# Performance work log

Hardware: AMD Instinct MI355X
Metric: run time of the kernel (lower is better)

## Reference

```python
import jax, jax.numpy as jnp
import numpy as np

B, H, W, D = 8, 64, 64, 1024


def setup_inputs() -> dict:
    key = jax.random.key(0)
    ks = jax.random.split(key, 10)
    s = 0.02
    return {
        "x": jax.random.normal(ks[0], (B, H, W, D), dtype=jnp.float32),
        "Wq": jax.random.normal(ks[1], (D, D), dtype=jnp.float32) * s,
        "bq": jnp.zeros((D,), dtype=jnp.float32),
        "Wk": jax.random.normal(ks[2], (D, D), dtype=jnp.float32) * s,
        "bk": jnp.zeros((D,), dtype=jnp.float32),
        "Wv": jax.random.normal(ks[3], (D, D), dtype=jnp.float32) * s,
        "bv": jnp.zeros((D,), dtype=jnp.float32),
        "Wo": jax.random.normal(ks[4], (D, D), dtype=jnp.float32) * s,
        "bo": jnp.zeros((D,), dtype=jnp.float32),
        "sigma": jnp.ones((1,), dtype=jnp.float32),
    }


def _dist(n, dtype):
    i = jnp.arange(n)
    return jnp.square(i[:, None] - i[None, :]).astype(dtype)


def reference(x, Wq, bq, Wk, bk, Wv, bv, Wo, bo, sigma):
    b, h, w, d = x.shape
    gw = 1.0 / (2.0 * jnp.square(sigma))  # scalar (shape [1])
    q = jnp.einsum('bhwd,ed->bhwe', x, Wq) + bq
    k = jnp.einsum('bhwd,ed->bhwe', x, Wk) + bk
    v = jnp.einsum('bhwd,ed->bhwe', x, Wv) + bv
    # row attention: attend across width within each row
    r_qk = jnp.einsum('bhwd,bhkd->bhwk', q, k) - gw[0] * _dist(w, x.dtype)
    r_attn = jax.nn.softmax(r_qk, axis=-1)               # [b,h,w,w]
    r_out = jnp.einsum('bhwk,bhkd->bhwd', r_attn, v)
    # column attention: attend across height within each column
    c_qk = jnp.einsum('bhwd,bgwd->bwhg', q, k) - gw[0] * _dist(h, x.dtype)
    c_attn = jax.nn.softmax(c_qk, axis=-1)               # [b,w,h,h]
    c_out = jnp.einsum('bwhg,bgwd->bhwd', c_attn, v)
    out = r_out + c_out
    return jnp.einsum('bhwd,ed->bhwe', out, Wo) + bo
```

## Files before the change

### kernel.cpp

```cpp
#include <hip/hip_runtime.h>


typedef _Float16 f16;
typedef __attribute__((ext_vector_type(8))) _Float16 f16x8;
typedef __attribute__((ext_vector_type(4))) float f32x4;

#define DEV __device__ __forceinline__

__global__ __launch_bounds__(256) void k_cvt_f16(const float* __restrict__ in,
                                                 f16* __restrict__ out, int n8) {
  int stride = gridDim.x * blockDim.x;
  for (int i = blockIdx.x * blockDim.x + threadIdx.x; i < n8; i += stride) {
    const float4* p = (const float4*)in + (size_t)i * 2;
    float4 a = p[0];
    float4 b = p[1];
    f16x8 o;
    o[0] = (f16)a.x; o[1] = (f16)a.y; o[2] = (f16)a.z; o[3] = (f16)a.w;
    o[4] = (f16)b.x; o[5] = (f16)b.y; o[6] = (f16)b.z; o[7] = (f16)b.w;
    *(f16x8*)(out + (size_t)i * 8) = o;
  }
}

template<bool C_F32>
__global__ __launch_bounds__(512, 2) void k_gemm256(const f16* __restrict__ A,
                                                    const f16* __restrict__ B,
                                                    const float* __restrict__ b0,
                                                    const float* __restrict__ b1,
                                                    const float* __restrict__ b2,
                                                    void* __restrict__ Cout,
                                                    int M, int N, int K) {
  __shared__ f16 smem[2][2][2][128 * 64];

  const int tid = threadIdx.x;
  const int lane = tid & 63;
  const int wid = tid >> 6;
  const int wr = wid >> 2;
  const int wc = wid & 3;
  const int lane_r = lane & 15;
  const int g = lane >> 4;

  const int nwg = gridDim.x;
  const int bid = blockIdx.x;
  const int swz = (bid & 7) * (nwg >> 3) + (bid >> 3);
  const int nbn = N >> 8;
  const int bm = swz / nbn, bn = swz % nbn;

  const int u0 = ((g) ^ (lane_r & 7)) * 8;
  const int u1 = ((4 + g) ^ (lane_r & 7)) * 8;
  const int arow = lane >> 3;
  const int acol = ((lane & 7) ^ (lane >> 3)) * 8;

  const f16* Ag[2] = { A + (size_t)(bm * 256) * K, A + (size_t)(bm * 256 + 128) * K };
  const f16* Bg[2] = { B + (size_t)(bn * 256) * K, B + (size_t)(bn * 256 + 128) * K };

  f32x4 acc[8][4];
#pragma unroll
  for (int i = 0; i < 8; ++i)
#pragma unroll
    for (int j = 0; j < 4; ++j) acc[i][j] = (f32x4){0.f, 0.f, 0.f, 0.f};

#define STAGE(gbase, kt, lbase)                                                     \
  {                                                                                 \
    _Pragma("unroll") for (int i_ = 0; i_ < 2; ++i_) {                              \
      const f16* g_ = (gbase) + (size_t)(wid * 16 + i_ * 8 + arow) * K + (kt) * 64 + acol; \
      __builtin_amdgcn_global_load_lds(                                             \
          (const __attribute__((address_space(1))) void*)g_,                        \
          (__attribute__((address_space(3))) void*)((lbase) + (wid * 16 + i_ * 8) * 64), \
          16, 0, 0);                                                                \
    }                                                                               \
  }

#define MFMAQ(q)                                                                    \
  _Pragma("unroll") for (int mm = 0; mm < 2; ++mm)                                  \
  _Pragma("unroll") for (int n = 0; n < 4; ++n) {                                   \
    acc[(q)*2 + mm][n] = __builtin_amdgcn_mfma_f32_16x16x32_f16(afrag[mm][0], bfrag[n][0], acc[(q)*2 + mm][n], 0, 0, 0); \
    acc[(q)*2 + mm][n] = __builtin_amdgcn_mfma_f32_16x16x32_f16(afrag[mm][1], bfrag[n][1], acc[(q)*2 + mm][n], 0, 0, 0); \
  }

#define READ_A(q)                                                                   \
  _Pragma("unroll") for (int mm = 0; mm < 2; ++mm) {                                \
    const int rb_ = ((q)*32 + mm * 16 + lane_r) * 64;                               \
    afrag[mm][0] = *(const f16x8*)&As_[rb_ + u0];                                   \
    afrag[mm][1] = *(const f16x8*)&As_[rb_ + u1];                                   \
  }

#define KTILE(t, slot, mode)                                                        \
  {                                                                                 \
    f16* As_ = smem[slot][0][wr];                                                   \
    f16* Bs_ = smem[slot][1][wc >> 1];                                              \
    f16x8 bfrag[4][2], afrag[2][2];                                                 \
    _Pragma("unroll") for (int n = 0; n < 4; ++n) {                                 \
      const int rb_ = ((wc & 1) * 64 + n * 16 + lane_r) * 64;                       \
      bfrag[n][0] = *(const f16x8*)&Bs_[rb_ + u0];                                  \
      bfrag[n][1] = *(const f16x8*)&Bs_[rb_ + u1];                                  \
    }                                                                               \
    READ_A(0)                                                                       \
    if ((mode) >= 1) STAGE(Ag[0], (t) + 1, smem[(slot) ^ 1][0][0]);                 \
    asm volatile("s_waitcnt lgkmcnt(8)" ::: "memory");                              \
    __builtin_amdgcn_s_barrier();                                                   \
    asm volatile("s_waitcnt lgkmcnt(0)" ::: "memory");                              \
    __builtin_amdgcn_s_setprio(1);                                                  \
    MFMAQ(0)                                                                        \
    __builtin_amdgcn_s_setprio(0);                                                  \
    __builtin_amdgcn_s_barrier();                                                   \
    READ_A(1)                                                                       \
    if ((mode) >= 1) STAGE(Ag[1], (t) + 1, smem[(slot) ^ 1][0][1]);                 \
    __builtin_amdgcn_s_barrier();                                                   \
    asm volatile("s_waitcnt lgkmcnt(0)" ::: "memory");                              \
    __builtin_amdgcn_s_setprio(1);                                                  \
    MFMAQ(1)                                                                        \
    __builtin_amdgcn_s_setprio(0);                                                  \
    __builtin_amdgcn_s_barrier();                                                   \
    READ_A(2)                                                                       \
    if ((mode) == 2) STAGE(Bg[0], (t) + 2, smem[slot][1][0]);                       \
    __builtin_amdgcn_s_barrier();                                                   \
    asm volatile("s_waitcnt lgkmcnt(0)" ::: "memory");                              \
    __builtin_amdgcn_s_setprio(1);                                                  \
    MFMAQ(2)                                                                        \
    __builtin_amdgcn_s_setprio(0);                                                  \
    __builtin_amdgcn_s_barrier();                                                   \
    READ_A(3)                                                                       \
    if ((mode) == 2) STAGE(Bg[1], (t) + 2, smem[slot][1][1]);                       \
    if ((mode) == 2) { asm volatile("s_waitcnt vmcnt(4)" ::: "memory"); }           \
    else if ((mode) == 1) { asm volatile("s_waitcnt vmcnt(0)" ::: "memory"); }      \
    __builtin_amdgcn_s_barrier();                                                   \
    asm volatile("s_waitcnt lgkmcnt(0)" ::: "memory");                              \
    __builtin_amdgcn_s_setprio(1);                                                  \
    MFMAQ(3)                                                                        \
    __builtin_amdgcn_s_setprio(0);                                                  \
    __builtin_amdgcn_s_barrier();                                                   \
  }

  const int nt = K >> 6;

  STAGE(Ag[0], 0, smem[0][0][0]);
  STAGE(Ag[1], 0, smem[0][0][1]);
  STAGE(Bg[0], 0, smem[0][1][0]);
  STAGE(Bg[1], 0, smem[0][1][1]);
  STAGE(Bg[0], 1, smem[1][1][0]);
  STAGE(Bg[1], 1, smem[1][1][1]);
  asm volatile("s_waitcnt vmcnt(4)" ::: "memory");
  __builtin_amdgcn_s_barrier();

  for (int t = 0; t + 3 < nt; t += 2) {
    KTILE(t, 0, 2)
    KTILE(t + 1, 1, 2)
  }
  KTILE(nt - 2, 0, 1)
  KTILE(nt - 1, 1, 0)

  const int mrow0 = bm * 256 + wr * 128 + (lane >> 4) * 4;
  const int ncol0 = bn * 256 + wc * 64 + (lane & 15);
#pragma unroll
  for (int n = 0; n < 4; ++n) {
    const int col = ncol0 + n * 16;
    const float* bp = (col < 1024) ? b0 : ((col < 2048) ? b1 : b2);
    const float bvv = bp[col & 1023];
#pragma unroll
    for (int mrep = 0; mrep < 8; ++mrep) {
#pragma unroll
      for (int r = 0; r < 4; ++r) {
        const int row = mrow0 + mrep * 16 + r;
        const float val = acc[mrep][n][r] + bvv;
        if (C_F32) ((float*)Cout)[(size_t)row * N + col] = val;
        else       ((f16*)Cout)[(size_t)row * N + col] = (f16)val;
      }
    }
  }
#undef KTILE
#undef READ_A
#undef MFMAQ
#undef STAGE
}

template<bool IS_COL>
__global__ __launch_bounds__(256) void k_attn(const f16* __restrict__ qkv,
                                              f16* __restrict__ attn,
                                              const float* __restrict__ sigma) {
  __shared__ union { float S[64][68]; f16 Vt[256][72]; } sm;
  __shared__ f16 P[64][72];

  const int tid = threadIdx.x;
  const int lane = tid & 63;
  const int wid = tid >> 6;
  const int blk = blockIdx.x;

  size_t tok0; int tstr;
  if (IS_COL) { tok0 = (size_t)(blk >> 6) * 4096 + (blk & 63); tstr = 64; }
  else        { tok0 = (size_t)blk * 64;                       tstr = 1;  }
  const size_t ibase = tok0 * 3072;  const int  istr = tstr * 3072;
  const size_t obase = tok0 * 1024;  const int  ostr = tstr * 1024;

  const float sg = sigma[0];
  const float gw = 0.5f / (sg * sg);

  const int m0 = wid * 16;
  const int lr = lane & 15;
  const int lq = lane >> 4;

  f32x4 sacc[4];
#pragma unroll
  for (int nt = 0; nt < 4; ++nt) sacc[nt] = (f32x4){0.f, 0.f, 0.f, 0.f};
  const f16* qp = qkv + ibase + (size_t)(m0 + lr) * istr + lq * 8;
  const f16* kp = qkv + ibase + 1024 + (size_t)lr * istr + lq * 8;
#pragma unroll 2
  for (int ks = 0; ks < 32; ++ks) {
    f16x8 af = *(const f16x8*)(qp + ks * 32);
#pragma unroll
    for (int nt = 0; nt < 4; ++nt) {
      f16x8 bfr = *(const f16x8*)(kp + (size_t)nt * 16 * istr + ks * 32);
      sacc[nt] = __builtin_amdgcn_mfma_f32_16x16x32_f16(af, bfr, sacc[nt], 0, 0, 0);
    }
  }
#pragma unroll
  for (int nt = 0; nt < 4; ++nt)
#pragma unroll
    for (int r = 0; r < 4; ++r) {
      const int row = m0 + lq * 4 + r;
      const int col = nt * 16 + lr;
      const float dd = (float)(row - col);
      sm.S[row][col] = sacc[nt][r] - gw * dd * dd;
    }
  __syncthreads();

  {
    const int r = tid >> 2, s4 = tid & 3;
    const float4* sp = (const float4*)&sm.S[r][s4 * 16];
    float vals[16];
#pragma unroll
    for (int j = 0; j < 4; ++j) {
      float4 t = sp[j];
      vals[j * 4 + 0] = t.x; vals[j * 4 + 1] = t.y; vals[j * 4 + 2] = t.z; vals[j * 4 + 3] = t.w;
    }
    float mx = vals[0];
#pragma unroll
    for (int j = 1; j < 16; ++j) mx = fmaxf(mx, vals[j]);
    mx = fmaxf(mx, __shfl_xor(mx, 1));
    mx = fmaxf(mx, __shfl_xor(mx, 2));
    float sum = 0.f;
#pragma unroll
    for (int j = 0; j < 16; ++j) { vals[j] = __expf(vals[j] - mx); sum += vals[j]; }
    sum += __shfl_xor(sum, 1);
    sum += __shfl_xor(sum, 2);
    const float inv = 1.f / sum;
#pragma unroll
    for (int j = 0; j < 16; ++j) P[r][s4 * 16 + j] = (f16)(vals[j] * inv);
  }
  __syncthreads();

  const f16x8 af0 = *(const f16x8*)&P[m0 + lr][lq * 8];
  const f16x8 af1 = *(const f16x8*)&P[m0 + lr][32 + lq * 8];

  const int kr = tid & 63;
  const int cg = tid >> 6;
  const f16* vp = qkv + ibase + 2048 + (size_t)kr * istr;

  for (int c = 0; c < 4; ++c) {
#pragma unroll
    for (int j8 = 0; j8 < 8; ++j8) {
      const int cl = cg * 64 + j8 * 8;
      f16x8 vv = *(const f16x8*)(vp + c * 256 + cl);
#pragma unroll
      for (int e = 0; e < 8; ++e) sm.Vt[cl + e][kr] = vv[e];
    }
    __syncthreads();
#pragma unroll
    for (int nt = 0; nt < 16; ++nt) {
      const f16x8 bf0 = *(const f16x8*)&sm.Vt[nt * 16 + lr][lq * 8];
      const f16x8 bf1 = *(const f16x8*)&sm.Vt[nt * 16 + lr][32 + lq * 8];
      f32x4 o = (f32x4){0.f, 0.f, 0.f, 0.f};
      o = __builtin_amdgcn_mfma_f32_16x16x32_f16(af0, bf0, o, 0, 0, 0);
      o = __builtin_amdgcn_mfma_f32_16x16x32_f16(af1, bf1, o, 0, 0, 0);
#pragma unroll
      for (int r = 0; r < 4; ++r) {
        const int row = m0 + lq * 4 + r;
        const int col = c * 256 + nt * 16 + lr;
        const size_t addr = obase + (size_t)row * ostr + col;
        float val = o[r];
        if (IS_COL) val += (float)attn[addr];
        attn[addr] = (f16)val;
      }
    }
    __syncthreads();
  }
}

extern "C" void kernel_launch(void* const* d_in, const int* in_sizes, int n_in,
                              void* d_out, int out_size, void* d_ws, size_t ws_size,
                              hipStream_t stream) {
  const float* x  = (const float*)d_in[0];
  const float* Wq = (const float*)d_in[1];
  const float* bq = (const float*)d_in[2];
  const float* Wk = (const float*)d_in[3];
  const float* bk = (const float*)d_in[4];
  const float* Wv = (const float*)d_in[5];
  const float* bv = (const float*)d_in[6];
  const float* Wo = (const float*)d_in[7];
  const float* bo = (const float*)d_in[8];
  const float* sg = (const float*)d_in[9];

  const int M = 8 * 64 * 64;
  const size_t NE = (size_t)M * 1024;

  f16* xb   = (f16*)d_ws;
  f16* wqkv = xb + NE;
  f16* wob  = wqkv + 3 * 1024 * 1024;
  f16* qkv  = wob + 1024 * 1024;

  k_cvt_f16<<<2048, 256, 0, stream>>>(x, xb, (int)(NE / 8));
  k_cvt_f16<<<256, 256, 0, stream>>>(Wq, wqkv,                   (1024 * 1024) / 8);
  k_cvt_f16<<<256, 256, 0, stream>>>(Wk, wqkv + 1024 * 1024,     (1024 * 1024) / 8);
  k_cvt_f16<<<256, 256, 0, stream>>>(Wv, wqkv + 2 * 1024 * 1024, (1024 * 1024) / 8);
  k_cvt_f16<<<256, 256, 0, stream>>>(Wo, wob,                    (1024 * 1024) / 8);

  k_gemm256<false><<<(M / 256) * (3072 / 256), 512, 0, stream>>>(
      xb, wqkv, bq, bk, bv, qkv, M, 3072, 1024);

  f16* attn = xb;
  k_attn<false><<<512, 256, 0, stream>>>(qkv, attn, sg);
  k_attn<true><<<512, 256, 0, stream>>>(qkv, attn, sg);

  k_gemm256<true><<<(M / 256) * (1024 / 256), 512, 0, stream>>>(
      attn, wob, bo, bo, bo, (float*)d_out, M, 1024, 1024);
}
```

Measured before the change: 523.6 us.

## Make GEMM persistent with cross-tile prefetch and merge conversion kernels

Turns the 256x256 GEMM into a persistent kernel with 256 workgroups, each looping over several output tiles. The next tile's first K-slices are prefetched during the last K-steps of the current tile, hiding the prologue and epilogue load latency. The five fp32-to-fp16 conversion launches are merged into one kernel to cut launch overhead. In exchange, the bid-swizzled tile ordering (bid&7 interleave) is dropped, which may hurt L2 reuse, and the epilogue stores are no longer overlapped across tiles.

```diff
diff --git a/kernel.cpp b/kernel.cpp
--- a/kernel.cpp
+++ b/kernel.cpp
@@ -5,19 +5,31 @@
 typedef __attribute__((ext_vector_type(8))) _Float16 f16x8;
 typedef __attribute__((ext_vector_type(4))) float f32x4;
 
-#define DEV __device__ __forceinline__
-
-__global__ __launch_bounds__(256) void k_cvt_f16(const float* __restrict__ in,
-                                                 f16* __restrict__ out, int n8) {
-  int stride = gridDim.x * blockDim.x;
-  for (int i = blockIdx.x * blockDim.x + threadIdx.x; i < n8; i += stride) {
-    const float4* p = (const float4*)in + (size_t)i * 2;
-    float4 a = p[0];
-    float4 b = p[1];
+__global__ __launch_bounds__(256) void k_cvt_all(
+    const float* __restrict__ x, const float* __restrict__ Wq,
+    const float* __restrict__ Wk, const float* __restrict__ Wv,
+    const float* __restrict__ Wo, f16* __restrict__ xb,
+    f16* __restrict__ wqkv, f16* __restrict__ wob) {
+  const int stride = gridDim.x * blockDim.x;
+  const int X8 = 33554432 / 8;
+  const int W8 = 1048576 / 8;
+  const int total = X8 + 4 * W8;
+  for (int i = blockIdx.x * blockDim.x + threadIdx.x; i < total; i += stride) {
+    const float* src; f16* dst; int o8;
+    if (i < X8) { src = x; dst = xb; o8 = i; }
+    else {
+      int j = i - X8; int seg = j >> 17; o8 = j & (W8 - 1);
+      if (seg == 0)      { src = Wq; dst = wqkv; }
+      else if (seg == 1) { src = Wk; dst = wqkv + 1048576; }
+      else if (seg == 2) { src = Wv; dst = wqkv + 2097152; }
+      else               { src = Wo; dst = wob; }
+    }
+    const float4* p = (const float4*)src + (size_t)o8 * 2;
+    float4 a = p[0]; float4 b = p[1];
     f16x8 o;
-    o[0] = (f16)a.x; o[1] = (f16)a.y; o[2] = (f16)a.z; o[3] = (f16)a.w;
-    o[4] = (f16)b.x; o[5] = (f16)b.y; o[6] = (f16)b.z; o[7] = (f16)b.w;
-    *(f16x8*)(out + (size_t)i * 8) = o;
+    o[0]=(f16)a.x; o[1]=(f16)a.y; o[2]=(f16)a.z; o[3]=(f16)a.w;
+    o[4]=(f16)b.x; o[5]=(f16)b.y; o[6]=(f16)b.z; o[7]=(f16)b.w;
+    *(f16x8*)(dst + (size_t)o8 * 8) = o;
   }
 }
 
@@ -28,7 +40,7 @@
                                                     const float* __restrict__ b1,
                                                     const float* __restrict__ b2,
                                                     void* __restrict__ Cout,
-                                                    int M, int N, int K) {
+                                                    int M, int N, int K, int ntiles) {
   __shared__ f16 smem[2][2][2][128 * 64];
 
   const int tid = threadIdx.x;
@@ -39,19 +51,10 @@
   const int lane_r = lane & 15;
   const int g = lane >> 4;
 
-  const int nwg = gridDim.x;
-  const int bid = blockIdx.x;
-  const int swz = (bid & 7) * (nwg >> 3) + (bid >> 3);
-  const int nbn = N >> 8;
-  const int bm = swz / nbn, bn = swz % nbn;
-
   const int u0 = ((g) ^ (lane_r & 7)) * 8;
   const int u1 = ((4 + g) ^ (lane_r & 7)) * 8;
   const int arow = lane >> 3;
   const int acol = ((lane & 7) ^ (lane >> 3)) * 8;
-
-  const f16* Ag[2] = { A + (size_t)(bm * 256) * K, A + (size_t)(bm * 256 + 128) * K };
-  const f16* Bg[2] = { B + (size_t)(bn * 256) * K, B + (size_t)(bn * 256 + 128) * K };
 
   f32x4 acc[8][4];
 #pragma unroll
@@ -84,7 +87,7 @@
     afrag[mm][1] = *(const f16x8*)&As_[rb_ + u1];                                   \
   }
 
-#define KTILE(t, slot, mode)                                                        \
+#define KTILE(slot, mode, AgP0, AgP1, ktA, BgP0, BgP1, ktB)                         \
   {                                                                                 \
     f16* As_ = smem[slot][0][wr];                                                   \
     f16* Bs_ = smem[slot][1][wc >> 1];                                              \
@@ -95,7 +98,7 @@
       bfrag[n][1] = *(const f16x8*)&Bs_[rb_ + u1];                                  \
     }                                                                               \
     READ_A(0)                                                                       \
-    if ((mode) >= 1) STAGE(Ag[0], (t) + 1, smem[(slot) ^ 1][0][0]);                 \
+    if ((mode) >= 1) STAGE(AgP0, ktA, smem[(slot) ^ 1][0][0]);                      \
     asm volatile("s_waitcnt lgkmcnt(8)" ::: "memory");                              \
     __builtin_amdgcn_s_barrier();                                                   \
     asm volatile("s_waitcnt lgkmcnt(0)" ::: "memory");                              \
@@ -104,7 +107,7 @@
     __builtin_amdgcn_s_setprio(0);                                                  \
     __builtin_amdgcn_s_barrier();                                                   \
     READ_A(1)                                                                       \
-    if ((mode) >= 1) STAGE(Ag[1], (t) + 1, smem[(slot) ^ 1][0][1]);                 \
+    if ((mode) >= 1) STAGE(AgP1, ktA, smem[(slot) ^ 1][0][1]);                      \
     __builtin_amdgcn_s_barrier();                                                   \
     asm volatile("s_waitcnt lgkmcnt(0)" ::: "memory");                              \
     __builtin_amdgcn_s_setprio(1);                                                  \
@@ -112,7 +115,7 @@
     __builtin_amdgcn_s_setprio(0);                                                  \
     __builtin_amdgcn_s_barrier();                                                   \
     READ_A(2)                                                                       \
-    if ((mode) == 2) STAGE(Bg[0], (t) + 2, smem[slot][1][0]);                       \
+    if ((mode) == 2) STAGE(BgP0, ktB, smem[slot][1][0]);                            \
     __builtin_amdgcn_s_barrier();                                                   \
     asm volatile("s_waitcnt lgkmcnt(0)" ::: "memory");                              \
     __builtin_amdgcn_s_setprio(1);                                                  \
@@ -120,7 +123,7 @@
     __builtin_amdgcn_s_setprio(0);                                                  \
     __builtin_amdgcn_s_barrier();                                                   \
     READ_A(3)                                                                       \
-    if ((mode) == 2) STAGE(Bg[1], (t) + 2, smem[slot][1][1]);                       \
+    if ((mode) == 2) STAGE(BgP1, ktB, smem[slot][1][1]);                            \
     if ((mode) == 2) { asm volatile("s_waitcnt vmcnt(4)" ::: "memory"); }           \
     else if ((mode) == 1) { asm volatile("s_waitcnt vmcnt(0)" ::: "memory"); }      \
     __builtin_amdgcn_s_barrier();                                                   \
@@ -131,41 +134,68 @@
     __builtin_amdgcn_s_barrier();                                                   \
   }
 
-  const int nt = K >> 6;
-
-  STAGE(Ag[0], 0, smem[0][0][0]);
-  STAGE(Ag[1], 0, smem[0][0][1]);
-  STAGE(Bg[0], 0, smem[0][1][0]);
-  STAGE(Bg[1], 0, smem[0][1][1]);
-  STAGE(Bg[0], 1, smem[1][1][0]);
-  STAGE(Bg[1], 1, smem[1][1][1]);
+  const int nbn = N >> 8;
+  const int NT = K >> 6;
+
+  int tidx = blockIdx.x;
+  const f16 *AgC0, *AgC1, *BgC0, *BgC1;
+  {
+    int bm = tidx / nbn, bn = tidx % nbn;
+    AgC0 = A + (size_t)(bm * 256) * K;  AgC1 = AgC0 + (size_t)128 * K;
+    BgC0 = B + (size_t)(bn * 256) * K;  BgC1 = BgC0 + (size_t)128 * K;
+  }
+
+  STAGE(AgC0, 0, smem[0][0][0]);
+  STAGE(AgC1, 0, smem[0][0][1]);
+  STAGE(BgC0, 0, smem[0][1][0]);
+  STAGE(BgC1, 0, smem[0][1][1]);
+  STAGE(BgC0, 1, smem[1][1][0]);
+  STAGE(BgC1, 1, smem[1][1][1]);
   asm volatile("s_waitcnt vmcnt(4)" ::: "memory");
   __builtin_amdgcn_s_barrier();
 
-  for (int t = 0; t + 3 < nt; t += 2) {
-    KTILE(t, 0, 2)
-    KTILE(t + 1, 1, 2)
-  }
-  KTILE(nt - 2, 0, 1)
-  KTILE(nt - 1, 1, 0)
-
-  const int mrow0 = bm * 256 + wr * 128 + (lane >> 4) * 4;
-  const int ncol0 = bn * 256 + wc * 64 + (lane & 15);
-#pragma unroll
-  for (int n = 0; n < 4; ++n) {
-    const int col = ncol0 + n * 16;
-    const float* bp = (col < 1024) ? b0 : ((col < 2048) ? b1 : b2);
-    const float bvv = bp[col & 1023];
-#pragma unroll
-    for (int mrep = 0; mrep < 8; ++mrep) {
-#pragma unroll
-      for (int r = 0; r < 4; ++r) {
-        const int row = mrow0 + mrep * 16 + r;
-        const float val = acc[mrep][n][r] + bvv;
-        if (C_F32) ((float*)Cout)[(size_t)row * N + col] = val;
-        else       ((f16*)Cout)[(size_t)row * N + col] = (f16)val;
+  for (int i = 0; i < ntiles; ++i) {
+    const f16 *AgN0 = AgC0, *AgN1 = AgC1, *BgN0 = BgC0, *BgN1 = BgC1;
+    const int nidx = tidx + gridDim.x;
+    if (i + 1 < ntiles) {
+      int bm = nidx / nbn, bn = nidx % nbn;
+      AgN0 = A + (size_t)(bm * 256) * K;  AgN1 = AgN0 + (size_t)128 * K;
+      BgN0 = B + (size_t)(bn * 256) * K;  BgN1 = BgN0 + (size_t)128 * K;
+    }
+    for (int t = 0; t + 3 < NT; t += 2) {
+      KTILE(0, 2, AgC0, AgC1, t + 1, BgC0, BgC1, t + 2)
+      KTILE(1, 2, AgC0, AgC1, t + 2, BgC0, BgC1, t + 3)
+    }
+    if (i + 1 < ntiles) {
+      KTILE(0, 2, AgC0, AgC1, NT - 1, BgN0, BgN1, 0)
+      KTILE(1, 2, AgN0, AgN1, 0,      BgN0, BgN1, 1)
+    } else {
+      KTILE(0, 1, AgC0, AgC1, NT - 1, BgC0, BgC1, 0)
+      KTILE(1, 0, AgC0, AgC1, 0,      BgC0, BgC1, 0)
+    }
+    {
+      const int bm = tidx / nbn, bn = tidx % nbn;
+      const int mrow0 = bm * 256 + wr * 128 + (lane >> 4) * 4;
+      const int ncol0 = bn * 256 + wc * 64 + (lane & 15);
+#pragma unroll
+      for (int n = 0; n < 4; ++n) {
+        const int col = ncol0 + n * 16;
+        const float* bp = (col < 1024) ? b0 : ((col < 2048) ? b1 : b2);
+        const float bvv = bp[col & 1023];
+#pragma unroll
+        for (int mrep = 0; mrep < 8; ++mrep) {
+#pragma unroll
+          for (int r = 0; r < 4; ++r) {
+            const int row = mrow0 + mrep * 16 + r;
+            const float val = acc[mrep][n][r] + bvv;
+            if (C_F32) ((float*)Cout)[(size_t)row * N + col] = val;
+            else       ((f16*)Cout)[(size_t)row * N + col] = (f16)val;
+            acc[mrep][n][r] = 0.f;
+          }
+        }
       }
     }
+    tidx = nidx; AgC0 = AgN0; AgC1 = AgN1; BgC0 = BgN0; BgC1 = BgN1;
   }
 #undef KTILE
 #undef READ_A
@@ -188,8 +218,8 @@
   size_t tok0; int tstr;
   if (IS_COL) { tok0 = (size_t)(blk >> 6) * 4096 + (blk & 63); tstr = 64; }
   else        { tok0 = (size_t)blk * 64;                       tstr = 1;  }
-  const size_t ibase = tok0 * 3072;  const int  istr = tstr * 3072;
-  const size_t obase = tok0 * 1024;  const int  ostr = tstr * 1024;
+  const size_t ibase = tok0 * 3072;  const int istr = tstr * 3072;
+  const size_t obase = tok0 * 1024;  const int ostr = tstr * 1024;
 
   const float sg = sigma[0];
   const float gw = 0.5f / (sg * sg);
@@ -307,19 +337,13 @@
   f16* wob  = wqkv + 3 * 1024 * 1024;
   f16* qkv  = wob + 1024 * 1024;
 
-  k_cvt_f16<<<2048, 256, 0, stream>>>(x, xb, (int)(NE / 8));
-  k_cvt_f16<<<256, 256, 0, stream>>>(Wq, wqkv,                   (1024 * 1024) / 8);
-  k_cvt_f16<<<256, 256, 0, stream>>>(Wk, wqkv + 1024 * 1024,     (1024 * 1024) / 8);
-  k_cvt_f16<<<256, 256, 0, stream>>>(Wv, wqkv + 2 * 1024 * 1024, (1024 * 1024) / 8);
-  k_cvt_f16<<<256, 256, 0, stream>>>(Wo, wob,                    (1024 * 1024) / 8);
-
-  k_gemm256<false><<<(M / 256) * (3072 / 256), 512, 0, stream>>>(
-      xb, wqkv, bq, bk, bv, qkv, M, 3072, 1024);
+  k_cvt_all<<<2048, 256, 0, stream>>>(x, Wq, Wk, Wv, Wo, xb, wqkv, wob);
+
+  k_gemm256<false><<<256, 512, 0, stream>>>(xb, wqkv, bq, bk, bv, qkv, M, 3072, 1024, 6);
 
   f16* attn = xb;
   k_attn<false><<<512, 256, 0, stream>>>(qkv, attn, sg);
   k_attn<true><<<512, 256, 0, stream>>>(qkv, attn, sg);
 
-  k_gemm256<true><<<(M / 256) * (1024 / 256), 512, 0, stream>>>(
-      attn, wob, bo, bo, bo, (float*)d_out, M, 1024, 1024);
+  k_gemm256<true><<<256, 512, 0, stream>>>(attn, wob, bo, bo, bo, (float*)d_out, M, 1024, 1024, 2);
 }
```

Result: slower. 657.8 us (+25.6%).
